# Kernel tuning notes

Hardware: AMD Instinct MI355X
Metric: run time of the kernel (lower is better)

The kernel has to match this reference:

```python
import jax, jax.numpy as jnp
import numpy as np

B, LQ, D, H, L, P, DFF = 16, 1024, 256, 8, 4, 4, 1024
SHAPES = ((64, 64), (32, 32), (16, 16), (8, 8))  # (H_l, W_l) per level
LV = sum(h * w for h, w in SHAPES)  # 5440
DH = D // H
EPS = 1e-5


def layer_norm(x, g, b):
    m = jnp.mean(x, -1, keepdims=True)
    v = jnp.mean((x - m) ** 2, -1, keepdims=True)
    return (x - m) * jax.lax.rsqrt(v + EPS) * g + b


def mha(q_in, k_in, v_in, w, b, ow, ob):
    # torch nn.MultiheadAttention with packed in_proj [3D, D]
    q = (q_in @ w[:D].T + b[:D]).reshape(B, LQ, H, DH)
    k = (k_in @ w[D:2 * D].T + b[D:2 * D]).reshape(B, LQ, H, DH)
    v = (v_in @ w[2 * D:].T + b[2 * D:]).reshape(B, LQ, H, DH)
    a = jax.nn.softmax(jnp.einsum('bqhd,bkhd->bhqk', q, k) * (1.0 / np.sqrt(DH)), -1)
    o = jnp.einsum('bhqk,bkhd->bqhd', a, v).reshape(B, LQ, D)
    return o @ ow.T + ob


def ms_deform_attn(q, ref, src, value_w, value_b, off_w, off_b, attw_w, attw_b, outp_w, outp_b):
    # value: [B, H, LV, DH]
    value = (src @ value_w.T + value_b).reshape(B, LV, H, DH).transpose(0, 2, 1, 3)
    off = (q @ off_w.T + off_b).reshape(B, LQ, H, L, P, 2)
    attw = jax.nn.softmax((q @ attw_w.T + attw_b).reshape(B, LQ, H, L * P), -1).reshape(B, LQ, H, L, P)
    # offset normalizer = (W_l, H_l) matching (x, y) order of reference points
    normalizer = jnp.array([[w, h] for h, w in SHAPES], jnp.float32)
    loc = ref[:, :, None, :, None, :] + off / normalizer[None, None, None, :, None, :]  # [B,LQ,H,L,P,2]
    out = jnp.zeros((B, LQ, H, DH), jnp.float32)
    start = 0
    for l, (hl, wl) in enumerate(SHAPES):
        v = value[:, :, start:start + hl * wl]  # [B,H,N_l,DH]
        start += hl * wl
        # grid_sample semantics, align_corners=False, padding zeros
        x = loc[:, :, :, l, :, 0] * wl - 0.5  # [B,LQ,H,P]
        y = loc[:, :, :, l, :, 1] * hl - 0.5
        x0 = jnp.floor(x); y0 = jnp.floor(y)
        lx = (x - x0).transpose(0, 2, 1, 3)[..., None]  # [B,H,LQ,P,1]
        ly = (y - y0).transpose(0, 2, 1, 3)[..., None]
        x0i = x0.astype(jnp.int32); y0i = y0.astype(jnp.int32)

        def gather(xi, yi):
            valid = ((xi >= 0) & (xi < wl) & (yi >= 0) & (yi < hl)).astype(jnp.float32)
            idx = jnp.clip(yi, 0, hl - 1) * wl + jnp.clip(xi, 0, wl - 1)  # [B,LQ,H,P]
            idx2 = idx.transpose(0, 2, 1, 3).reshape(B, H, LQ * P)
            g = jnp.take_along_axis(v, jnp.broadcast_to(idx2[..., None], (B, H, LQ * P, DH)), axis=2)
            return g.reshape(B, H, LQ, P, DH) * valid.transpose(0, 2, 1, 3)[..., None]

        g00 = gather(x0i, y0i); g01 = gather(x0i + 1, y0i)
        g10 = gather(x0i, y0i + 1); g11 = gather(x0i + 1, y0i + 1)
        sampled = (g00 * (1 - lx) * (1 - ly) + g01 * lx * (1 - ly)
                   + g10 * (1 - lx) * ly + g11 * lx * ly)  # [B,H,LQ,P,DH]
        out = out + jnp.einsum('bhqpd,bqhp->bqhd', sampled, attw[:, :, :, l])
    return out.reshape(B, LQ, D) @ outp_w.T + outp_b


def setup_inputs() -> dict:
    key = jax.random.key(0)
    ks = jax.random.split(key, 16)
    s = 0.02
    inp = {}
    inp['tgt'] = jax.random.normal(ks[0], (B, LQ, D), jnp.float32)
    inp['query_pos'] = jax.random.normal(ks[1], (B, LQ, D), jnp.float32)
    inp['reference_points'] = jax.random.uniform(ks[2], (B, LQ, L, 2), jnp.float32)
    inp['src'] = jax.random.normal(ks[3], (B, LV, D), jnp.float32)
    # self-attention (MHA)
    inp['in_proj_w'] = jax.random.normal(ks[4], (3 * D, D), jnp.float32) * s
    inp['in_proj_b'] = jnp.zeros((3 * D,), jnp.float32)
    inp['out_proj_w'] = jax.random.normal(ks[5], (D, D), jnp.float32) * s
    inp['out_proj_b'] = jnp.zeros((D,), jnp.float32)
    inp['norm2_g'] = jnp.ones((D,), jnp.float32); inp['norm2_b'] = jnp.zeros((D,), jnp.float32)
    # MSDeformAttn
    inp['value_w'] = jax.random.normal(ks[6], (D, D), jnp.float32) * s
    inp['value_b'] = jnp.zeros((D,), jnp.float32)
    inp['off_w'] = jax.random.normal(ks[7], (H * L * P * 2, D), jnp.float32) * s
    inp['off_b'] = jax.random.normal(ks[8], (H * L * P * 2,), jnp.float32) * 0.5
    inp['attw_w'] = jax.random.normal(ks[9], (H * L * P, D), jnp.float32) * s
    inp['attw_b'] = jnp.zeros((H * L * P,), jnp.float32)
    inp['outp_w'] = jax.random.normal(ks[10], (D, D), jnp.float32) * s
    inp['outp_b'] = jnp.zeros((D,), jnp.float32)
    inp['norm1_g'] = jnp.ones((D,), jnp.float32); inp['norm1_b'] = jnp.zeros((D,), jnp.float32)
    # FFN
    inp['lin1_w'] = jax.random.normal(ks[11], (DFF, D), jnp.float32) * s
    inp['lin1_b'] = jnp.zeros((DFF,), jnp.float32)
    inp['lin2_w'] = jax.random.normal(ks[12], (D, DFF), jnp.float32) * s
    inp['lin2_b'] = jnp.zeros((D,), jnp.float32)
    inp['norm3_g'] = jnp.ones((D,), jnp.float32); inp['norm3_b'] = jnp.zeros((D,), jnp.float32)
    inp['src_spatial_shapes'] = jnp.array(SHAPES, jnp.int32)
    inp['level_start_index'] = jnp.array(np.concatenate([[0], np.cumsum([h * w for h, w in SHAPES[:-1]])]), jnp.int32)
    return inp


def reference(tgt, query_pos, reference_points, src,
              in_proj_w, in_proj_b, out_proj_w, out_proj_b, norm2_g, norm2_b,
              value_w, value_b, off_w, off_b, attw_w, attw_b, outp_w, outp_b,
              norm1_g, norm1_b, lin1_w, lin1_b, lin2_w, lin2_b, norm3_g, norm3_b,
              src_spatial_shapes, level_start_index):
    # dropout=0 (eval mode)
    q = tgt + query_pos
    tgt2 = mha(q, q, tgt, in_proj_w, in_proj_b, out_proj_w, out_proj_b)
    tgt = layer_norm(tgt + tgt2, norm2_g, norm2_b)
    tgt2 = ms_deform_attn(tgt + query_pos, reference_points, src,
                          value_w, value_b, off_w, off_b, attw_w, attw_b, outp_w, outp_b)
    tgt = layer_norm(tgt + tgt2, norm1_g, norm1_b)
    t2 = jax.nn.relu(tgt @ lin1_w.T + lin1_b) @ lin2_w.T + lin2_b
    return layer_norm(tgt + t2, norm3_g, norm3_b)
```

## Files before the change

kernel.cpp:

```cpp
#include <hip/hip_runtime.h>
#include <math.h>

typedef short s16x8 __attribute__((ext_vector_type(8)));
typedef float f32x4 __attribute__((ext_vector_type(4)));
typedef unsigned short u16;
typedef unsigned short u16x4 __attribute__((ext_vector_type(4)));
typedef unsigned short u16x8 __attribute__((ext_vector_type(8)));

constexpr int cB    = 16;
constexpr int cLQ   = 1024;
constexpr int cD    = 256;
constexpr int cH    = 8;
constexpr int cLVTOT= 5440;
constexpr int cNTOK = cB * cLQ;
constexpr int cNV   = cB * cLVTOT;

__device__ __forceinline__ u16 f2b(float f) {
    __bf16 h = (__bf16)f;
    u16 u;
    __builtin_memcpy(&u, &h, 2);
    return u;
}
__device__ __forceinline__ float bl(unsigned x) {
    return __uint_as_float(x << 16);
}
__device__ __forceinline__ u16x8 cvt8(float4 a, float4 b) {
    return (u16x8){ f2b(a.x), f2b(a.y), f2b(a.z), f2b(a.w),
                    f2b(b.x), f2b(b.y), f2b(b.z), f2b(b.w) };
}

struct WArgs { const float4* src[8]; };
__global__ __launch_bounds__(256) void prep_all(const float4* __restrict__ t,
                                                const float4* __restrict__ q,
                                                u16x8* __restrict__ tb,
                                                u16x8* __restrict__ qb,
                                                const float4* __restrict__ src,
                                                u16x8* __restrict__ srcb,
                                                WArgs wa,
                                                u16x8* __restrict__ wout,
                                                const float* __restrict__ off_b,
                                                const float* __restrict__ attw_b,
                                                float* __restrict__ biasoa) {
    int bid = blockIdx.x;
    if (bid < 1024) {
        size_t u = (size_t)bid * 256 + threadIdx.x;
        const float4* tp = t + u * 4;
        const float4* qp = q + u * 4;
        float4 a0 = tp[0], a1 = tp[1], a2 = tp[2], a3 = tp[3];
        float4 b0 = qp[0], b1 = qp[1], b2 = qp[2], b3 = qp[3];
        tb[u * 2]     = cvt8(a0, a1);
        tb[u * 2 + 1] = cvt8(a2, a3);
        float4 s0 = {a0.x + b0.x, a0.y + b0.y, a0.z + b0.z, a0.w + b0.w};
        float4 s1 = {a1.x + b1.x, a1.y + b1.y, a1.z + b1.z, a1.w + b1.w};
        float4 s2 = {a2.x + b2.x, a2.y + b2.y, a2.z + b2.z, a2.w + b2.w};
        float4 s3 = {a3.x + b3.x, a3.y + b3.y, a3.z + b3.z, a3.w + b3.w};
        qb[u * 2]     = cvt8(s0, s1);
        qb[u * 2 + 1] = cvt8(s2, s3);
    } else if (bid < 6464) {
        size_t u = (size_t)(bid - 1024) * 256 + threadIdx.x;
        const float4* sp = src + u * 4;
        float4 a0 = sp[0], a1 = sp[1], a2 = sp[2], a3 = sp[3];
        srcb[u * 2]     = cvt8(a0, a1);
        srcb[u * 2 + 1] = cvt8(a2, a3);
    } else if (bid < 6712) {
        int u = (bid - 6464) * 256 + threadIdx.x;
        int i = u * 4;
        int s, off;
        if (i < 98304) {
            if (i < 65536) { if (i < 49152) { s = 0; off = i; } else { s = 1; off = i - 49152; } }
            else           { if (i < 81920) { s = 2; off = i - 65536; } else { s = 3; off = i - 81920; } }
        } else {
            if (i < 122880){ if (i < 106496){ s = 4; off = i - 98304; } else { s = 5; off = i - 106496; } }
            else           { if (i < 188416){ s = 6; off = i - 122880; } else { s = 7; off = i - 188416; } }
        }
        const float4* wp = wa.src[s] + off;
        float4 a0 = wp[0], a1 = wp[1], a2 = wp[2], a3 = wp[3];
        wout[(size_t)u * 2]     = cvt8(a0, a1);
        wout[(size_t)u * 2 + 1] = cvt8(a2, a3);
    } else {
        int tix = threadIdx.x;
        biasoa[tix] = off_b[tix];
        if (tix < 128) biasoa[256 + tix] = attw_b[tix];
    }
}

__global__ __launch_bounds__(256) void gemm_qkv_val(const u16* __restrict__ A0,
                                                    const u16* __restrict__ A1,
                                                    const u16* __restrict__ Wt,
                                                    const float* __restrict__ bias,
                                                    u16* __restrict__ QKb,
                                                    u16* __restrict__ Vtg,
                                                    const u16* __restrict__ Av,
                                                    const u16* __restrict__ Wv,
                                                    const float* __restrict__ bv,
                                                    u16* __restrict__ Cv) {
    __shared__ u16 As[128 * 32];
    __shared__ u16 Bs[128 * 32];
    const int K = 256;
    int tid = threadIdx.x;
    int bid = blockIdx.x;
    int w = tid >> 6, lane = tid & 63, quad = lane >> 4, l15 = lane & 15;
    int wm = (w & 1) * 64, wn = (w >> 1) * 64;
    int isval = bid < 1360;
    int bm, bn;
    const u16 *A, *W;
    const float* bp;
    if (isval) {
        bm = (bid % 680) * 128; bn = (bid / 680) * 128;
        A = Av; W = Wv; bp = bv;
    } else {
        int id = bid - 1360;
        bm = (id & 127) * 128;
        int by = id >> 7;
        bn = by * 128;
        A = (by < 4) ? A0 : A1;
        W = Wt; bp = bias;
    }
    int r0 = tid >> 2;
    int c0 = ((tid & 3) ^ ((tid >> 3) & 3)) * 8;
    const u16* ga0 = A + (size_t)(bm + r0) * K + c0;
    const u16* ga1 = ga0 + (size_t)64 * K;
    const u16* gb0 = W + (size_t)(bn + r0) * K + c0;
    const u16* gb1 = gb0 + (size_t)64 * K;
    int abk = (quad ^ ((l15 >> 1) & 3)) * 8;
    f32x4 acc[16];
#pragma unroll
    for (int i = 0; i < 16; ++i) acc[i] = (f32x4){0.f, 0.f, 0.f, 0.f};
    s16x8 ra0 = *(const s16x8*)ga0, ra1 = *(const s16x8*)ga1;
    s16x8 rb0 = *(const s16x8*)gb0, rb1 = *(const s16x8*)gb1;
#pragma unroll 2
    for (int i = 0; i < 8; ++i) {
        *(s16x8*)&As[tid * 8]        = ra0;
        *(s16x8*)&As[2048 + tid * 8] = ra1;
        *(s16x8*)&Bs[tid * 8]        = rb0;
        *(s16x8*)&Bs[2048 + tid * 8] = rb1;
        __syncthreads();
        if (i < 7) {
            int k1 = (i + 1) << 5;
            ra0 = *(const s16x8*)(ga0 + k1); ra1 = *(const s16x8*)(ga1 + k1);
            rb0 = *(const s16x8*)(gb0 + k1); rb1 = *(const s16x8*)(gb1 + k1);
        }
        s16x8 af[4], bf[4];
#pragma unroll
        for (int mt = 0; mt < 4; ++mt) af[mt] = *(const s16x8*)&As[(wm + mt * 16 + l15) * 32 + abk];
#pragma unroll
        for (int nt = 0; nt < 4; ++nt) bf[nt] = *(const s16x8*)&Bs[(wn + nt * 16 + l15) * 32 + abk];
#pragma unroll
        for (int mt = 0; mt < 4; ++mt)
#pragma unroll
            for (int nt = 0; nt < 4; ++nt)
                acc[mt * 4 + nt] = __builtin_amdgcn_mfma_f32_16x16x32_bf16(af[mt], bf[nt], acc[mt * 4 + nt], 0, 0, 0);
        __syncthreads();
    }
    float bs[4];
#pragma unroll
    for (int nt = 0; nt < 4; ++nt) bs[nt] = bp[bn + wn + nt * 16 + l15];
    if (isval) {
#pragma unroll
        for (int mt = 0; mt < 4; ++mt) {
            int m = bm + wm + mt * 16 + quad * 4;
#pragma unroll
            for (int nt = 0; nt < 4; ++nt) {
                int n = bn + wn + nt * 16 + l15;
#pragma unroll
                for (int r = 0; r < 4; ++r)
                    Cv[(size_t)(m + r) * 256 + n] = f2b(acc[mt * 4 + nt][r] + bs[nt]);
            }
        }
    } else if (bn < 512) {
        float qs = (bn + wn < 256) ? 0.25506734f : 1.0f;
#pragma unroll
        for (int mt = 0; mt < 4; ++mt) {
            int m = bm + wm + mt * 16 + quad * 4;
#pragma unroll
            for (int nt = 0; nt < 4; ++nt) {
                int n = bn + wn + nt * 16 + l15;
#pragma unroll
                for (int r = 0; r < 4; ++r)
                    QKb[(size_t)(m + r) * 512 + n] = f2b((acc[mt * 4 + nt][r] + bs[nt]) * qs);
            }
        }
    } else {
#pragma unroll
        for (int mt = 0; mt < 4; ++mt) {
            int m = bm + wm + mt * 16 + quad * 4;
            int b = m >> 10, t = m & 1023;
#pragma unroll
            for (int nt = 0; nt < 4; ++nt) {
                int nv = bn + wn + nt * 16 + l15 - 512;
                int h = nv >> 5, dh = nv & 31;
                u16x4 o;
#pragma unroll
                for (int r = 0; r < 4; ++r) o[r] = f2b(acc[mt * 4 + nt][r] + bs[nt]);
                *(u16x4*)(Vtg + (((size_t)(b * 8 + h) * 32 + dh) << 10) + t) = o;
            }
        }
    }
}

template <int RELU, int OUTBF>
__global__ __launch_bounds__(256) void gemm128(const u16* __restrict__ A,
                                               const u16* __restrict__ Wt,
                                               const float* __restrict__ bias,
                                               float* __restrict__ Cf,
                                               u16* __restrict__ Cb,
                                               int M, int N, int K) {
    __shared__ u16 As[128 * 32];
    __shared__ u16 Bs[128 * 32];
    int tid = threadIdx.x;
    int bm = blockIdx.x * 128, bn = blockIdx.y * 128;
    int w = tid >> 6, lane = tid & 63, quad = lane >> 4, l15 = lane & 15;
    int wm = (w & 1) * 64, wn = (w >> 1) * 64;
    int r0 = tid >> 2;
    int c0 = ((tid & 3) ^ ((tid >> 3) & 3)) * 8;
    const u16* ga0 = A  + (size_t)(bm + r0) * K + c0;
    const u16* ga1 = ga0 + (size_t)64 * K;
    const u16* gb0 = Wt + (size_t)(bn + r0) * K + c0;
    const u16* gb1 = gb0 + (size_t)64 * K;
    int abk = (quad ^ ((l15 >> 1) & 3)) * 8;
    f32x4 acc[16];
#pragma unroll
    for (int i = 0; i < 16; ++i) acc[i] = (f32x4){0.f, 0.f, 0.f, 0.f};
    s16x8 ra0 = *(const s16x8*)ga0, ra1 = *(const s16x8*)ga1;
    s16x8 rb0 = *(const s16x8*)gb0, rb1 = *(const s16x8*)gb1;
    int nk = K >> 5;
#pragma unroll 2
    for (int i = 0; i < nk; ++i) {
        *(s16x8*)&As[tid * 8]        = ra0;
        *(s16x8*)&As[2048 + tid * 8] = ra1;
        *(s16x8*)&Bs[tid * 8]        = rb0;
        *(s16x8*)&Bs[2048 + tid * 8] = rb1;
        __syncthreads();
        if (i + 1 < nk) {
            int k1 = (i + 1) << 5;
            ra0 = *(const s16x8*)(ga0 + k1); ra1 = *(const s16x8*)(ga1 + k1);
            rb0 = *(const s16x8*)(gb0 + k1); rb1 = *(const s16x8*)(gb1 + k1);
        }
        s16x8 af[4], bf[4];
#pragma unroll
        for (int mt = 0; mt < 4; ++mt) af[mt] = *(const s16x8*)&As[(wm + mt * 16 + l15) * 32 + abk];
#pragma unroll
        for (int nt = 0; nt < 4; ++nt) bf[nt] = *(const s16x8*)&Bs[(wn + nt * 16 + l15) * 32 + abk];
#pragma unroll
        for (int mt = 0; mt < 4; ++mt)
#pragma unroll
            for (int nt = 0; nt < 4; ++nt)
                acc[mt * 4 + nt] = __builtin_amdgcn_mfma_f32_16x16x32_bf16(af[mt], bf[nt], acc[mt * 4 + nt], 0, 0, 0);
        __syncthreads();
    }
    float bs[4];
#pragma unroll
    for (int nt = 0; nt < 4; ++nt) bs[nt] = bias[bn + wn + nt * 16 + l15];
#pragma unroll
    for (int mt = 0; mt < 4; ++mt) {
        int m = bm + wm + mt * 16 + quad * 4;
#pragma unroll
        for (int nt = 0; nt < 4; ++nt) {
            int n = bn + wn + nt * 16 + l15;
#pragma unroll
            for (int r = 0; r < 4; ++r) {
                float v = acc[mt * 4 + nt][r] + bs[nt];
                if (RELU) v = fmaxf(v, 0.f);
                if (OUTBF) Cb[(size_t)(m + r) * N + n] = f2b(v);
                else       Cf[(size_t)(m + r) * N + n] = v;
            }
        }
    }
}

template <int RELU, int OUTBF>
__global__ __launch_bounds__(256) void gemm64(const u16* __restrict__ A,
                                              const u16* __restrict__ Wt,
                                              const float* __restrict__ bias,
                                              float* __restrict__ Cf,
                                              u16* __restrict__ Cb,
                                              int M, int N, int K) {
    __shared__ u16 As[64 * 32];
    __shared__ u16 Bs[128 * 32];
    int tid = threadIdx.x;
    int bm = blockIdx.x * 64, bn = blockIdx.y * 128;
    int w = tid >> 6, lane = tid & 63, quad = lane >> 4, l15 = lane & 15;
    int wn = w * 32;
    int r0 = tid >> 2;
    int c0 = ((tid & 3) ^ ((tid >> 3) & 3)) * 8;
    const u16* ga0 = A  + (size_t)(bm + r0) * K + c0;
    const u16* gb0 = Wt + (size_t)(bn + r0) * K + c0;
    const u16* gb1 = gb0 + (size_t)64 * K;
    int abk = (quad ^ ((l15 >> 1) & 3)) * 8;
    f32x4 acc[8];
#pragma unroll
    for (int i = 0; i < 8; ++i) acc[i] = (f32x4){0.f, 0.f, 0.f, 0.f};
    s16x8 ra0 = *(const s16x8*)ga0;
    s16x8 rb0 = *(const s16x8*)gb0, rb1 = *(const s16x8*)gb1;
    int nk = K >> 5;
#pragma unroll 2
    for (int i = 0; i < nk; ++i) {
        *(s16x8*)&As[tid * 8]        = ra0;
        *(s16x8*)&Bs[tid * 8]        = rb0;
        *(s16x8*)&Bs[2048 + tid * 8] = rb1;
        __syncthreads();
        if (i + 1 < nk) {
            int k1 = (i + 1) << 5;
            ra0 = *(const s16x8*)(ga0 + k1);
            rb0 = *(const s16x8*)(gb0 + k1); rb1 = *(const s16x8*)(gb1 + k1);
        }
        s16x8 af[4], bf[2];
#pragma unroll
        for (int mt = 0; mt < 4; ++mt) af[mt] = *(const s16x8*)&As[(mt * 16 + l15) * 32 + abk];
#pragma unroll
        for (int nt = 0; nt < 2; ++nt) bf[nt] = *(const s16x8*)&Bs[(wn + nt * 16 + l15) * 32 + abk];
#pragma unroll
        for (int mt = 0; mt < 4; ++mt)
#pragma unroll
            for (int nt = 0; nt < 2; ++nt)
                acc[mt * 2 + nt] = __builtin_amdgcn_mfma_f32_16x16x32_bf16(af[mt], bf[nt], acc[mt * 2 + nt], 0, 0, 0);
        __syncthreads();
    }
    float bs[2];
#pragma unroll
    for (int nt = 0; nt < 2; ++nt) bs[nt] = bias[bn + wn + nt * 16 + l15];
#pragma unroll
    for (int mt = 0; mt < 4; ++mt) {
        int m = bm + mt * 16 + quad * 4;
#pragma unroll
        for (int nt = 0; nt < 2; ++nt) {
            int n = bn + wn + nt * 16 + l15;
#pragma unroll
            for (int r = 0; r < 4; ++r) {
                float v = acc[mt * 2 + nt][r] + bs[nt];
                if (RELU) v = fmaxf(v, 0.f);
                if (OUTBF) Cb[(size_t)(m + r) * N + n] = f2b(v);
                else       Cf[(size_t)(m + r) * N + n] = v;
            }
        }
    }
}

__global__ __launch_bounds__(256) void attn_sw(const u16* __restrict__ QK,
                                               const u16* __restrict__ Vt,
                                               u16* __restrict__ O) {
    __shared__ __align__(16) u16 smem[8192];
    int tid = threadIdx.x, w = tid >> 6, lane = tid & 63, quad = lane >> 4, l15 = lane & 15;
    u16* Ks  = smem;
    u16* Vs  = smem + 2048;
    u16* Psw = smem + 4096 + w * 1024;
    int id = blockIdx.x;
    int qt = id & 15, bh = id >> 4;
    int h = bh & 7, b = bh >> 3;
    int qbase = qt * 64 + w * 16;
    s16x8 qf = *(const s16x8*)(QK + (size_t)(b * cLQ + qbase + l15) * 512 + h * 32 + quad * 8);
    f32x4 o0 = {0.f,0.f,0.f,0.f}, o1 = {0.f,0.f,0.f,0.f}, o2 = {0.f,0.f,0.f,0.f};
    int skey = tid >> 2, kchunk = tid & 3;
    int ks_off = skey * 32 + ((kchunk ^ ((skey >> 1) & 3)) * 8);
    int sdh = kchunk * 8;
    int vdh = tid >> 3, vchunk = tid & 7;
    int vs_off = vdh * 64 + ((vchunk ^ (vdh & 7)) * 8);
    int vkc = vchunk * 8;
    int ksw = (l15 >> 1) & 3;
    int vsw = l15 & 7;
    size_t kgbase = (size_t)(b * cLQ) * 512 + 256 + h * 32;
    size_t vgbase = (size_t)bh * 32 * cLQ;
    s16x8 kreg = *(const s16x8*)(QK + kgbase + (size_t)skey * 512 + sdh);
    s16x8 vreg = *(const s16x8*)(Vt + vgbase + (size_t)vdh * cLQ + vkc);
    const s16x8 ones = {16256,16256,16256,16256,16256,16256,16256,16256};
    for (int kt = 0; kt < cLQ; kt += 64) {
        __syncthreads();
        *(s16x8*)&Ks[ks_off] = kreg;
        *(s16x8*)&Vs[vs_off] = vreg;
        if (kt + 64 < cLQ) {
            kreg = *(const s16x8*)(QK + kgbase + (size_t)(kt + 64 + skey) * 512 + sdh);
            vreg = *(const s16x8*)(Vt + vgbase + (size_t)vdh * cLQ + kt + 64 + vkc);
        }
        __syncthreads();
#pragma unroll
        for (int t = 0; t < 4; ++t) {
            s16x8 kf = *(const s16x8*)&Ks[(t * 16 + l15) * 32 + (quad ^ ksw) * 8];
            f32x4 z = {0.f,0.f,0.f,0.f};
            f32x4 sc = __builtin_amdgcn_mfma_f32_16x16x32_bf16(kf, qf, z, 0, 0, 0);
            u16x4 pb;
#pragma unroll
            for (int r = 0; r < 4; ++r) pb[r] = f2b(exp2f(sc[r]));
            *(u16x4*)&Psw[l15 * 64 + (((t * 2 + (quad >> 1)) ^ vsw) * 8) + (quad & 1) * 4] = pb;
        }
#pragma unroll
        for (int ks = 0; ks < 2; ++ks) {
            int coff = ((ks * 4 + quad) ^ vsw) * 8;
            s16x8 pa  = *(const s16x8*)&Psw[l15 * 64 + coff];
            s16x8 vb0 = *(const s16x8*)&Vs[l15 * 64 + coff];
            s16x8 vb1 = *(const s16x8*)&Vs[(l15 + 16) * 64 + coff];
            o0 = __builtin_amdgcn_mfma_f32_16x16x32_bf16(pa, vb0, o0, 0, 0, 0);
            o1 = __builtin_amdgcn_mfma_f32_16x16x32_bf16(pa, vb1, o1, 0, 0, 0);
            o2 = __builtin_amdgcn_mfma_f32_16x16x32_bf16(pa, ones, o2, 0, 0, 0);
        }
    }
#pragma unroll
    for (int r = 0; r < 4; ++r) {
        float inv = 1.0f / o2[r];
        int q = qbase + quad * 4 + r;
        size_t ob = (size_t)(b * cLQ + q) * cD + h * 32;
        O[ob + l15]      = f2b(o0[r] * inv);
        O[ob + 16 + l15] = f2b(o1[r] * inv);
    }
}

template <int WB, int QP>
__global__ __launch_bounds__(256) void add_ln_kernel(const float* __restrict__ X,
                                                     const float* __restrict__ R,
                                                     const float* __restrict__ g,
                                                     const float* __restrict__ bt,
                                                     const float* __restrict__ qp,
                                                     float* __restrict__ out,
                                                     u16* __restrict__ outb) {
    int wave = threadIdx.x / 64;
    int lane = threadIdx.x % 64;
    int row = blockIdx.x * 4 + wave;
    const float* x = X + (size_t)row * cD;
    const float* r = R + (size_t)row * cD;
    float4 xv = *(const float4*)(x + lane * 4);
    float4 rv = *(const float4*)(r + lane * 4);
    float v0 = xv.x + rv.x, v1 = xv.y + rv.y, v2 = xv.z + rv.z, v3 = xv.w + rv.w;
    float s = v0 + v1 + v2 + v3;
    float s2 = v0 * v0 + v1 * v1 + v2 * v2 + v3 * v3;
#pragma unroll
    for (int off = 32; off > 0; off >>= 1) {
        s += __shfl_xor(s, off);
        s2 += __shfl_xor(s2, off);
    }
    float mean = s * (1.0f / 256.0f);
    float var = s2 * (1.0f / 256.0f) - mean * mean;
    float rstd = rsqrtf(var + 1e-5f);
    float4 gv = *(const float4*)(g + lane * 4);
    float4 bv = *(const float4*)(bt + lane * 4);
    float4 o;
    o.x = (v0 - mean) * rstd * gv.x + bv.x;
    o.y = (v1 - mean) * rstd * gv.y + bv.y;
    o.z = (v2 - mean) * rstd * gv.z + bv.z;
    o.w = (v3 - mean) * rstd * gv.w + bv.w;
    *(float4*)(out + (size_t)row * cD + lane * 4) = o;
    if (WB) {
        u16x4 ob = { f2b(o.x), f2b(o.y), f2b(o.z), f2b(o.w) };
        *(u16x4*)(outb + (size_t)row * cD + lane * 4) = ob;
    }
    if (QP) {
        float4 qv = *(const float4*)(qp + (size_t)row * cD + lane * 4);
        u16x4 ob = { f2b(o.x + qv.x), f2b(o.y + qv.y), f2b(o.z + qv.z), f2b(o.w + qv.w) };
        *(u16x4*)(outb + (size_t)row * cD + lane * 4) = ob;
    }
}

__global__ __launch_bounds__(256) void deform_kernel(const u16* __restrict__ value,
                                                     const float* __restrict__ oa,
                                                     const float* __restrict__ refp,
                                                     u16* __restrict__ out) {
    int t = blockIdx.x * 32 + (threadIdx.x >> 3);
    int dq = threadIdx.x & 7;
    int h = t & 7;
    int bq = t >> 3;
    int b = bq >> 10;
    const float* al = oa + (size_t)bq * 384 + 256 + h * 16;
    float wv[16];
    float mx = -1e30f;
#pragma unroll
    for (int i = 0; i < 16; ++i) { wv[i] = al[i]; mx = fmaxf(mx, wv[i]); }
    float sum = 0.f;
#pragma unroll
    for (int i = 0; i < 16; ++i) { wv[i] = __expf(wv[i] - mx); sum += wv[i]; }
    float inv = 1.f / sum;
    const float* off = oa + (size_t)bq * 384 + h * 32;
    const float* rp = refp + (size_t)bq * 8;
    const u16* vb = value + ((size_t)b * cLVTOT) * 256 + h * 32 + dq * 4;
    const int starts[4] = {0, 4096, 5120, 5376};
    const int dims[4] = {64, 32, 16, 8};
    float a0 = 0.f, a1 = 0.f, a2 = 0.f, a3 = 0.f;
#pragma unroll
    for (int l = 0; l < 4; ++l) {
        int hl = dims[l], wl = dims[l];
        float rx = rp[l * 2 + 0], ry = rp[l * 2 + 1];
#pragma unroll
        for (int p = 0; p < 4; ++p) {
            float ox = off[(l * 4 + p) * 2 + 0];
            float oy = off[(l * 4 + p) * 2 + 1];
            float x = rx * (float)wl + ox - 0.5f;
            float y = ry * (float)hl + oy - 0.5f;
            float x0f = floorf(x), y0f = floorf(y);
            float lx = x - x0f, ly = y - y0f;
            int x0 = (int)x0f, y0 = (int)y0f;
            float aw = wv[l * 4 + p] * inv;
            float cw[4] = {(1.f - lx) * (1.f - ly), lx * (1.f - ly),
                           (1.f - lx) * ly, lx * ly};
            int xs[4] = {x0, x0 + 1, x0, x0 + 1};
            int ys[4] = {y0, y0, y0 + 1, y0 + 1};
#pragma unroll
            for (int c = 0; c < 4; ++c) {
                int xi = xs[c], yi = ys[c];
                bool valid = (xi >= 0) && (xi < wl) && (yi >= 0) && (yi < hl);
                int xc = min(max(xi, 0), wl - 1);
                int yc = min(max(yi, 0), hl - 1);
                int idx = starts[l] + yc * wl + xc;
                float wgt = valid ? aw * cw[c] : 0.f;
                unsigned long long u = *(const unsigned long long*)(vb + (size_t)idx * 256);
                a0 += wgt * bl((unsigned)(u & 0xffffull));
                a1 += wgt * bl((unsigned)((u >> 16) & 0xffffull));
                a2 += wgt * bl((unsigned)((u >> 32) & 0xffffull));
                a3 += wgt * bl((unsigned)(u >> 48));
            }
        }
    }
    u16x4 o = { f2b(a0), f2b(a1), f2b(a2), f2b(a3) };
    *(u16x4*)(out + (size_t)bq * 256 + h * 32 + dq * 4) = o;
}

extern "C" void kernel_launch(void* const* d_in, const int* in_sizes, int n_in,
                              void* d_out, int out_size, void* d_ws, size_t ws_size,
                              hipStream_t stream) {
    const float* tgt        = (const float*)d_in[0];
    const float* query_pos  = (const float*)d_in[1];
    const float* refp       = (const float*)d_in[2];
    const float* src        = (const float*)d_in[3];
    const float* in_proj_w  = (const float*)d_in[4];
    const float* in_proj_b  = (const float*)d_in[5];
    const float* out_proj_b = (const float*)d_in[7];
    const float* norm2_g    = (const float*)d_in[8];
    const float* norm2_b    = (const float*)d_in[9];
    const float* value_b    = (const float*)d_in[11];
    const float* off_b      = (const float*)d_in[13];
    const float* attw_b     = (const float*)d_in[15];
    const float* outp_b     = (const float*)d_in[17];
    const float* norm1_g    = (const float*)d_in[18];
    const float* norm1_b    = (const float*)d_in[19];
    const float* lin1_b     = (const float*)d_in[21];
    const float* lin2_b     = (const float*)d_in[23];
    const float* norm3_g    = (const float*)d_in[24];
    const float* norm3_b    = (const float*)d_in[25];

    char* W = (char*)d_ws;
    const size_t S84 = 8388608;
    u16*   tgtb  = (u16*)(W + 0);
    u16*   q2b   = (u16*)(W + 0);
    u16*   qb    = (u16*)(W + 1 * S84);
    u16*   QKb   = (u16*)(W + 2 * S84);
    u16*   dtb   = (u16*)(W + 2 * S84);
    u16*   x2b   = (u16*)(W + 3 * S84);
    float* ffn2f = (float*)(W + 4 * S84);
    u16*   aob   = (u16*)(W + 5 * S84);
    float* oaf   = (float*)(W + 5 * S84);
    u16*   Vtg   = (u16*)(W + 6 * S84);
    float* t2f   = (float*)(W + 6 * S84);
    float* x1f   = (float*)(W + 8 * S84);
    float* x2f   = (float*)(W + 10 * S84);
    u16*   srcb  = (u16*)(W + 12 * S84);
    u16*   ffn1b = (u16*)(W + 12 * S84);
    u16*   valb  = (u16*)(W + 12 * S84 + 44564480);
    char*  wbase = W + 12 * S84 + 2 * 44564480;
    u16* wb_in   = (u16*)(wbase + 0);
    u16* wb_out  = (u16*)(wbase + 393216);
    u16* wb_val  = (u16*)(wbase + 524288);
    u16* wb_off  = (u16*)(wbase + 655360);
    u16* wb_outp = (u16*)(wbase + 851968);
    u16* wb_lin1 = (u16*)(wbase + 983040);
    u16* wb_lin2 = (u16*)(wbase + 1507328);
    float* biasoa= (float*)(wbase + 2031616);
    float* out = (float*)d_out;

    dim3 blk(256);

    WArgs wa;
    wa.src[0] = (const float4*)in_proj_w;  wa.src[1] = (const float4*)d_in[6];
    wa.src[2] = (const float4*)d_in[10];   wa.src[3] = (const float4*)d_in[12];
    wa.src[4] = (const float4*)d_in[14];   wa.src[5] = (const float4*)d_in[16];
    wa.src[6] = (const float4*)d_in[20];   wa.src[7] = (const float4*)d_in[22];
    prep_all<<<dim3(6713), blk, 0, stream>>>((const float4*)tgt, (const float4*)query_pos,
                                             (u16x8*)tgtb, (u16x8*)qb,
                                             (const float4*)src, (u16x8*)srcb,
                                             wa, (u16x8*)wb_in, off_b, attw_b, biasoa);

    gemm_qkv_val<<<dim3(2128), blk, 0, stream>>>(qb, tgtb, wb_in, in_proj_b, QKb, Vtg,
                                                 srcb, wb_val, value_b, valb);
    attn_sw<<<dim3(cB * cH * 16), blk, 0, stream>>>(QKb, Vtg, aob);
    gemm64<0, 0><<<dim3(256, 2), blk, 0, stream>>>(aob, wb_out, out_proj_b, t2f, nullptr, cNTOK, 256, 256);
    add_ln_kernel<0, 1><<<dim3(4096), blk, 0, stream>>>(tgt, t2f, norm2_g, norm2_b, query_pos, x1f, q2b);

    gemm64<0, 0><<<dim3(256, 3), blk, 0, stream>>>(q2b, wb_off, biasoa, oaf, nullptr, cNTOK, 384, 256);
    deform_kernel<<<dim3(4096), blk, 0, stream>>>(valb, oaf, refp, dtb);
    gemm64<0, 0><<<dim3(256, 2), blk, 0, stream>>>(dtb, wb_outp, outp_b, t2f, nullptr, cNTOK, 256, 256);
    add_ln_kernel<1, 0><<<dim3(4096), blk, 0, stream>>>(x1f, t2f, norm1_g, norm1_b, nullptr, x2f, x2b);

    gemm128<1, 1><<<dim3(128, 8), blk, 0, stream>>>(x2b, wb_lin1, lin1_b, nullptr, ffn1b, cNTOK, 1024, 256);
    gemm64<0, 0><<<dim3(256, 2), blk, 0, stream>>>(ffn1b, wb_lin2, lin2_b, ffn2f, nullptr, cNTOK, 256, 1024);
    add_ln_kernel<0, 0><<<dim3(4096), blk, 0, stream>>>(x2f, ffn2f, norm3_g, norm3_b, nullptr, out, nullptr);
}
```

Measured before the change: 440.7 us.

## Fuse src bf16 conversion into value GEMM and share deform sampling setup across lanes

```diff
diff --git a/kernel.cpp b/kernel.cpp
--- a/kernel.cpp
+++ b/kernel.cpp
@@ -34,8 +34,6 @@
                                                 const float4* __restrict__ q,
                                                 u16x8* __restrict__ tb,
                                                 u16x8* __restrict__ qb,
-                                                const float4* __restrict__ src,
-                                                u16x8* __restrict__ srcb,
                                                 WArgs wa,
                                                 u16x8* __restrict__ wout,
                                                 const float* __restrict__ off_b,
@@ -56,14 +54,8 @@
         float4 s3 = {a3.x + b3.x, a3.y + b3.y, a3.z + b3.z, a3.w + b3.w};
         qb[u * 2]     = cvt8(s0, s1);
         qb[u * 2 + 1] = cvt8(s2, s3);
-    } else if (bid < 6464) {
-        size_t u = (size_t)(bid - 1024) * 256 + threadIdx.x;
-        const float4* sp = src + u * 4;
-        float4 a0 = sp[0], a1 = sp[1], a2 = sp[2], a3 = sp[3];
-        srcb[u * 2]     = cvt8(a0, a1);
-        srcb[u * 2 + 1] = cvt8(a2, a3);
-    } else if (bid < 6712) {
-        int u = (bid - 6464) * 256 + threadIdx.x;
+    } else if (bid < 1272) {
+        int u = (bid - 1024) * 256 + threadIdx.x;
         int i = u * 4;
         int s, off;
         if (i < 98304) {
@@ -90,7 +82,7 @@
                                                     const float* __restrict__ bias,
                                                     u16* __restrict__ QKb,
                                                     u16* __restrict__ Vtg,
-                                                    const u16* __restrict__ Av,
+                                                    const float* __restrict__ Av,
                                                     const u16* __restrict__ Wv,
                                                     const float* __restrict__ bv,
                                                     u16* __restrict__ Cv) {
@@ -101,31 +93,72 @@
     int bid = blockIdx.x;
     int w = tid >> 6, lane = tid & 63, quad = lane >> 4, l15 = lane & 15;
     int wm = (w & 1) * 64, wn = (w >> 1) * 64;
-    int isval = bid < 1360;
-    int bm, bn;
-    const u16 *A, *W;
-    const float* bp;
-    if (isval) {
-        bm = (bid % 680) * 128; bn = (bid / 680) * 128;
-        A = Av; W = Wv; bp = bv;
-    } else {
-        int id = bid - 1360;
-        bm = (id & 127) * 128;
-        int by = id >> 7;
-        bn = by * 128;
-        A = (by < 4) ? A0 : A1;
-        W = Wt; bp = bias;
-    }
     int r0 = tid >> 2;
     int c0 = ((tid & 3) ^ ((tid >> 3) & 3)) * 8;
+    int abk = (quad ^ ((l15 >> 1) & 3)) * 8;
+    f32x4 acc[16];
+#pragma unroll
+    for (int i = 0; i < 16; ++i) acc[i] = (f32x4){0.f, 0.f, 0.f, 0.f};
+
+    if (bid < 1360) {
+        int bm = (bid >> 1) * 128, bn = (bid & 1) * 128;
+        const float* ga0 = Av + (size_t)(bm + r0) * 256 + c0;
+        const float* ga1 = ga0 + (size_t)64 * 256;
+        const u16* gb0 = Wv + (size_t)(bn + r0) * 256 + c0;
+        const u16* gb1 = gb0 + (size_t)64 * 256;
+        float4 ra0a = *(const float4*)ga0, ra0b = *(const float4*)(ga0 + 4);
+        float4 ra1a = *(const float4*)ga1, ra1b = *(const float4*)(ga1 + 4);
+        s16x8 rb0 = *(const s16x8*)gb0, rb1 = *(const s16x8*)gb1;
+#pragma unroll 2
+        for (int i = 0; i < 8; ++i) {
+            *(u16x8*)&As[tid * 8]        = cvt8(ra0a, ra0b);
+            *(u16x8*)&As[2048 + tid * 8] = cvt8(ra1a, ra1b);
+            *(s16x8*)&Bs[tid * 8]        = rb0;
+            *(s16x8*)&Bs[2048 + tid * 8] = rb1;
+            __syncthreads();
+            if (i < 7) {
+                int k1 = (i + 1) << 5;
+                ra0a = *(const float4*)(ga0 + k1); ra0b = *(const float4*)(ga0 + k1 + 4);
+                ra1a = *(const float4*)(ga1 + k1); ra1b = *(const float4*)(ga1 + k1 + 4);
+                rb0  = *(const s16x8*)(gb0 + k1);  rb1  = *(const s16x8*)(gb1 + k1);
+            }
+            s16x8 af[4], bf[4];
+#pragma unroll
+            for (int mt = 0; mt < 4; ++mt) af[mt] = *(const s16x8*)&As[(wm + mt * 16 + l15) * 32 + abk];
+#pragma unroll
+            for (int nt = 0; nt < 4; ++nt) bf[nt] = *(const s16x8*)&Bs[(wn + nt * 16 + l15) * 32 + abk];
+#pragma unroll
+            for (int mt = 0; mt < 4; ++mt)
+#pragma unroll
+                for (int nt = 0; nt < 4; ++nt)
+                    acc[mt * 4 + nt] = __builtin_amdgcn_mfma_f32_16x16x32_bf16(af[mt], bf[nt], acc[mt * 4 + nt], 0, 0, 0);
+            __syncthreads();
+        }
+        float bs[4];
+#pragma unroll
+        for (int nt = 0; nt < 4; ++nt) bs[nt] = bv[bn + wn + nt * 16 + l15];
+#pragma unroll
+        for (int mt = 0; mt < 4; ++mt) {
+            int m = bm + wm + mt * 16 + quad * 4;
+#pragma unroll
+            for (int nt = 0; nt < 4; ++nt) {
+                int n = bn + wn + nt * 16 + l15;
+#pragma unroll
+                for (int r = 0; r < 4; ++r)
+                    Cv[(size_t)(m + r) * 256 + n] = f2b(acc[mt * 4 + nt][r] + bs[nt]);
+            }
+        }
+        return;
+    }
+    int id = bid - 1360;
+    int bm = (id & 127) * 128;
+    int by = id >> 7;
+    int bn = by * 128;
+    const u16* A = (by < 4) ? A0 : A1;
     const u16* ga0 = A + (size_t)(bm + r0) * K + c0;
     const u16* ga1 = ga0 + (size_t)64 * K;
-    const u16* gb0 = W + (size_t)(bn + r0) * K + c0;
+    const u16* gb0 = Wt + (size_t)(bn + r0) * K + c0;
     const u16* gb1 = gb0 + (size_t)64 * K;
-    int abk = (quad ^ ((l15 >> 1) & 3)) * 8;
-    f32x4 acc[16];
-#pragma unroll
-    for (int i = 0; i < 16; ++i) acc[i] = (f32x4){0.f, 0.f, 0.f, 0.f};
     s16x8 ra0 = *(const s16x8*)ga0, ra1 = *(const s16x8*)ga1;
     s16x8 rb0 = *(const s16x8*)gb0, rb1 = *(const s16x8*)gb1;
 #pragma unroll 2
@@ -154,20 +187,8 @@
     }
     float bs[4];
 #pragma unroll
-    for (int nt = 0; nt < 4; ++nt) bs[nt] = bp[bn + wn + nt * 16 + l15];
-    if (isval) {
-#pragma unroll
-        for (int mt = 0; mt < 4; ++mt) {
-            int m = bm + wm + mt * 16 + quad * 4;
-#pragma unroll
-            for (int nt = 0; nt < 4; ++nt) {
-                int n = bn + wn + nt * 16 + l15;
-#pragma unroll
-                for (int r = 0; r < 4; ++r)
-                    Cv[(size_t)(m + r) * 256 + n] = f2b(acc[mt * 4 + nt][r] + bs[nt]);
-            }
-        }
-    } else if (bn < 512) {
+    for (int nt = 0; nt < 4; ++nt) bs[nt] = bias[bn + wn + nt * 16 + l15];
+    if (bn < 512) {
         float qs = (bn + wn < 256) ? 0.25506734f : 1.0f;
 #pragma unroll
         for (int mt = 0; mt < 4; ++mt) {
@@ -468,42 +489,52 @@
     float inv = 1.f / sum;
     const float* off = oa + (size_t)bq * 384 + h * 32;
     const float* rp = refp + (size_t)bq * 8;
+    float wgtA[4], wgtB[4];
+    int   idxA[4], idxB[4];
+#pragma unroll
+    for (int k = 0; k < 2; ++k) {
+        int s = dq * 2 + k;
+        int l = s >> 2;
+        int dim = 64 >> l;
+        unsigned start = (16384u - (16384u >> (2 * l))) / 3u;
+        float ox = off[s * 2 + 0];
+        float oy = off[s * 2 + 1];
+        float x = rp[l * 2 + 0] * (float)dim + ox - 0.5f;
+        float y = rp[l * 2 + 1] * (float)dim + oy - 0.5f;
+        float x0f = floorf(x), y0f = floorf(y);
+        float lx = x - x0f, ly = y - y0f;
+        int x0 = (int)x0f, y0 = (int)y0f;
+        float aw = wv[s] * inv;
+        float cw[4] = {(1.f - lx) * (1.f - ly), lx * (1.f - ly),
+                       (1.f - lx) * ly, lx * ly};
+        int xs[4] = {x0, x0 + 1, x0, x0 + 1};
+        int ys[4] = {y0, y0, y0 + 1, y0 + 1};
+#pragma unroll
+        for (int c = 0; c < 4; ++c) {
+            int xi = xs[c], yi = ys[c];
+            bool valid = (xi >= 0) && (xi < dim) && (yi >= 0) && (yi < dim);
+            int xc = min(max(xi, 0), dim - 1);
+            int yc = min(max(yi, 0), dim - 1);
+            int ix = (int)start + yc * dim + xc;
+            float wg = valid ? aw * cw[c] : 0.f;
+            if (k == 0) { wgtA[c] = wg; idxA[c] = ix; }
+            else        { wgtB[c] = wg; idxB[c] = ix; }
+        }
+    }
     const u16* vb = value + ((size_t)b * cLVTOT) * 256 + h * 32 + dq * 4;
-    const int starts[4] = {0, 4096, 5120, 5376};
-    const int dims[4] = {64, 32, 16, 8};
     float a0 = 0.f, a1 = 0.f, a2 = 0.f, a3 = 0.f;
 #pragma unroll
-    for (int l = 0; l < 4; ++l) {
-        int hl = dims[l], wl = dims[l];
-        float rx = rp[l * 2 + 0], ry = rp[l * 2 + 1];
-#pragma unroll
-        for (int p = 0; p < 4; ++p) {
-            float ox = off[(l * 4 + p) * 2 + 0];
-            float oy = off[(l * 4 + p) * 2 + 1];
-            float x = rx * (float)wl + ox - 0.5f;
-            float y = ry * (float)hl + oy - 0.5f;
-            float x0f = floorf(x), y0f = floorf(y);
-            float lx = x - x0f, ly = y - y0f;
-            int x0 = (int)x0f, y0 = (int)y0f;
-            float aw = wv[l * 4 + p] * inv;
-            float cw[4] = {(1.f - lx) * (1.f - ly), lx * (1.f - ly),
-                           (1.f - lx) * ly, lx * ly};
-            int xs[4] = {x0, x0 + 1, x0, x0 + 1};
-            int ys[4] = {y0, y0, y0 + 1, y0 + 1};
-#pragma unroll
-            for (int c = 0; c < 4; ++c) {
-                int xi = xs[c], yi = ys[c];
-                bool valid = (xi >= 0) && (xi < wl) && (yi >= 0) && (yi < hl);
-                int xc = min(max(xi, 0), wl - 1);
-                int yc = min(max(yi, 0), hl - 1);
-                int idx = starts[l] + yc * wl + xc;
-                float wgt = valid ? aw * cw[c] : 0.f;
-                unsigned long long u = *(const unsigned long long*)(vb + (size_t)idx * 256);
-                a0 += wgt * bl((unsigned)(u & 0xffffull));
-                a1 += wgt * bl((unsigned)((u >> 16) & 0xffffull));
-                a2 += wgt * bl((unsigned)((u >> 32) & 0xffffull));
-                a3 += wgt * bl((unsigned)(u >> 48));
-            }
+    for (int s = 0; s < 16; ++s) {
+        int srcl = s >> 1;
+#pragma unroll
+        for (int c = 0; c < 4; ++c) {
+            float wgt = __shfl((s & 1) ? wgtB[c] : wgtA[c], srcl, 8);
+            int   idx = __shfl((s & 1) ? idxB[c] : idxA[c], srcl, 8);
+            unsigned long long u = *(const unsigned long long*)(vb + (size_t)idx * 256);
+            a0 += wgt * bl((unsigned)(u & 0xffffull));
+            a1 += wgt * bl((unsigned)((u >> 16) & 0xffffull));
+            a2 += wgt * bl((unsigned)((u >> 32) & 0xffffull));
+            a3 += wgt * bl((unsigned)(u >> 48));
         }
     }
     u16x4 o = { f2b(a0), f2b(a1), f2b(a2), f2b(a3) };
@@ -548,7 +579,6 @@
     float* t2f   = (float*)(W + 6 * S84);
     float* x1f   = (float*)(W + 8 * S84);
     float* x2f   = (float*)(W + 10 * S84);
-    u16*   srcb  = (u16*)(W + 12 * S84);
     u16*   ffn1b = (u16*)(W + 12 * S84);
     u16*   valb  = (u16*)(W + 12 * S84 + 44564480);
     char*  wbase = W + 12 * S84 + 2 * 44564480;
@@ -569,13 +599,12 @@
     wa.src[2] = (const float4*)d_in[10];   wa.src[3] = (const float4*)d_in[12];
     wa.src[4] = (const float4*)d_in[14];   wa.src[5] = (const float4*)d_in[16];
     wa.src[6] = (const float4*)d_in[20];   wa.src[7] = (const float4*)d_in[22];
-    prep_all<<<dim3(6713), blk, 0, stream>>>((const float4*)tgt, (const float4*)query_pos,
+    prep_all<<<dim3(1273), blk, 0, stream>>>((const float4*)tgt, (const float4*)query_pos,
                                              (u16x8*)tgtb, (u16x8*)qb,
-                                             (const float4*)src, (u16x8*)srcb,
                                              wa, (u16x8*)wb_in, off_b, attw_b, biasoa);
 
     gemm_qkv_val<<<dim3(2128), blk, 0, stream>>>(qb, tgtb, wb_in, in_proj_b, QKb, Vtg,
-                                                 srcb, wb_val, value_b, valb);
+                                                 src, wb_val, value_b, valb);
     attn_sw<<<dim3(cB * cH * 16), blk, 0, stream>>>(QKb, Vtg, aob);
     gemm64<0, 0><<<dim3(256, 2), blk, 0, stream>>>(aob, wb_out, out_proj_b, t2f, nullptr, cNTOK, 256, 256);
     add_ln_kernel<0, 1><<<dim3(4096), blk, 0, stream>>>(tgt, t2f, norm2_g, norm2_b, query_pos, x1f, q2b);
```

After: 425.6 us. 1.04x faster.
